# Optimization experiments

Hardware: AMD Instinct MI355X
Metric: run time of the kernel (lower is better)

The kernel has to match this reference:

```python
import jax, jax.numpy as jnp
import numpy as np

GRID = 64  # 64x64 key grid -> K = 4096


def setup_inputs() -> dict:
    key = jax.random.key(0)
    k1, k2, k3, k4 = jax.random.split(key, 4)
    B, H, Q, K, D = 2, 8, 2048, GRID * GRID, 128
    queries = jax.random.normal(k1, (B, H, Q, D), dtype=jnp.float32)
    keys = jax.random.normal(k2, (B, H, K, D), dtype=jnp.float32)
    # integer (x, y) query positions on the grid
    pos = jax.random.randint(k3, (B, Q, 2), 0, GRID).astype(jnp.int64)
    # relative bias table per head, offsets in [-(GRID-1), GRID-1]
    rel_bias = jax.random.normal(k4, (H, 2 * GRID - 1, 2 * GRID - 1), dtype=jnp.float32)
    # key grid coordinates (row-major flattened 64x64 grid)
    ar = jnp.arange(K)
    grid_x = (ar % GRID).astype(jnp.int64)
    grid_y = (ar // GRID).astype(jnp.int64)
    return {"queries": queries, "keys": keys, "pos": pos, "rel_bias": rel_bias,
            "grid_x": grid_x, "grid_y": grid_y}


def reference(queries, keys, pos, rel_bias, grid_x, grid_y):
    # queries: [B,H,Q,D], keys: [B,H,K,D], pos: [B,Q,2] int,
    # rel_bias: [H,2G-1,2G-1], grid_x/grid_y: [K] int
    D = queries.shape[-1]
    scale = jnp.asarray(1.0 / np.sqrt(D), dtype=queries.dtype)
    scores = jnp.einsum('bhqd,bhkd->bhqk', queries, keys) * scale  # [B,H,Q,K]
    Hb, Wb = rel_bias.shape[-2], rel_bias.shape[-1]
    cy, cx = (Hb - 1) // 2, (Wb - 1) // 2
    # relative offsets, shifted to table indices: [B,Q,K]
    dy = grid_y[None, None, :] - pos[:, :, 1][:, :, None] + cy
    dx = grid_x[None, None, :] - pos[:, :, 0][:, :, None] + cx
    dy = jnp.clip(dy, 0, Hb - 1)
    dx = jnp.clip(dx, 0, Wb - 1)
    flat = (dy * Wb + dx).astype(jnp.int32)  # [B,Q,K]
    # gather per-head bias: [H, B, Q, K] -> [B, H, Q, K]
    bias = jnp.take(rel_bias.reshape(rel_bias.shape[0], -1), flat, axis=1)
    scores = scores + jnp.transpose(bias, (1, 0, 2, 3))
    return jax.nn.softmax(scores, axis=-1)
```

## Files before the change

kernel.cpp:

```cpp
#include <hip/hip_runtime.h>
#include <hip/hip_bf16.h>

typedef __attribute__((ext_vector_type(8))) short short8;
typedef __attribute__((ext_vector_type(4))) float f32x4;

constexpr int Bn = 2, Hn = 8, NQ = 2048, NK = 4096, Dd = 128, Wt = 127;
constexpr int QT = 64, KT = 64;
constexpr int SPLITS = 8, K1_TILES = 8, NC2 = 4;
constexpr int NROWS = Bn * Hn * NQ;
constexpr float SCALE = 0.08838834764831845f;
constexpr float LOG2E = 1.4426950408889634f;
constexpr float S2 = SCALE * LOG2E;
constexpr float BSHIFT = 12.0f * LOG2E;

constexpr size_t WS_SUMS = 0;
constexpr size_t WS_K = 1u << 20;
constexpr size_t WS_Q = WS_K + (size_t)Bn * Hn * NK * Dd * 2;
constexpr size_t WS_B = WS_Q + (size_t)Bn * Hn * NQ * Dd * 2;

constexpr int KELEM = Bn * Hn * NK * Dd;
constexpr int QELEM = Bn * Hn * NQ * Dd;
constexpr int BELEM = Hn * Wt * Wt;
constexpr int KBLK = KELEM / 2048;
constexpr int QBLK = QELEM / 2048;
constexpr int BBLK = (BELEM + 2047) / 2048;

__device__ __forceinline__ short bf16r(float f) {
  union { float f; unsigned u; } v; v.f = f;
  unsigned r = v.u + 0x7fffu + ((v.u >> 16) & 1u);
  return (short)(r >> 16);
}

__device__ __forceinline__ float exp2hw(float x) {
  float r;
  asm("v_exp_f32 %0, %1" : "=v"(r) : "v"(x));
  return r;
}

__global__ __launch_bounds__(256)
void prep_kernel(const float* __restrict__ Km, const float* __restrict__ Qm,
                 const float* __restrict__ Bias, short* __restrict__ wsK,
                 short* __restrict__ wsQ, float* __restrict__ wsB) {
  const int bid = blockIdx.x, tid = threadIdx.x;
  if (bid < KBLK) {
    size_t i = (size_t)bid * 2048 + tid * 8;
    float4 f0 = *(const float4*)(Km + i);
    float4 f1 = *(const float4*)(Km + i + 4);
    short8 v;
    v[0] = bf16r(f0.x); v[1] = bf16r(f0.y); v[2] = bf16r(f0.z); v[3] = bf16r(f0.w);
    v[4] = bf16r(f1.x); v[5] = bf16r(f1.y); v[6] = bf16r(f1.z); v[7] = bf16r(f1.w);
    *(short8*)(wsK + i) = v;
  } else if (bid < KBLK + QBLK) {
    size_t i = (size_t)(bid - KBLK) * 2048 + tid * 8;
    float4 f0 = *(const float4*)(Qm + i);
    float4 f1 = *(const float4*)(Qm + i + 4);
    short8 v;
    v[0] = bf16r(f0.x); v[1] = bf16r(f0.y); v[2] = bf16r(f0.z); v[3] = bf16r(f0.w);
    v[4] = bf16r(f1.x); v[5] = bf16r(f1.y); v[6] = bf16r(f1.z); v[7] = bf16r(f1.w);
    *(short8*)(wsQ + i) = v;
  } else {
    int i = (bid - KBLK - QBLK) * 2048 + tid * 8;
#pragma unroll
    for (int j = 0; j < 8; j++)
      if (i + j < BELEM) wsB[i + j] = Bias[i + j] * LOG2E - BSHIFT;
  }
}

__device__ __forceinline__ void stage_async(int tid, const short* __restrict__ kp,
                                            int kt0, short* buf) {
  const int wave = tid >> 6, lane = tid & 63;
#pragma unroll
  for (int c = 0; c < 4; c++) {
    const int db = c * 4096 + wave * 1024 + lane * 16;
    const int row = db >> 8;
    const int scol = ((db >> 4) & 15) ^ (row & 7);
    const short* src = kp + (size_t)(kt0 + row) * Dd + scol * 8;
    __builtin_amdgcn_global_load_lds(
        (const __attribute__((address_space(1))) void*)src,
        (__attribute__((address_space(3))) void*)(buf + ((c * 4096 + wave * 1024) >> 1)),
        16, 0, 0);
  }
}

__device__ __forceinline__ short8 loadKfrag(const short* buf, int f, int kc,
                                            int l15, int g) {
  const int krow = f * 16 + l15;
  const int byte = (krow << 8) + ((((kc << 2) + g) ^ (krow & 7)) << 4);
  return *(const short8*)((const char*)buf + byte);
}

__global__ __launch_bounds__(256, 4)
void rga_sum_kernel(const short* __restrict__ wsK, const short* __restrict__ wsQ,
                    const int* __restrict__ Pos, const float* __restrict__ wsB,
                    float* __restrict__ sums) {
  __shared__ short lds[2][KT * Dd];
  const int tid = threadIdx.x, wave = tid >> 6, lane = tid & 63;
  const int l15 = lane & 15, g = lane >> 4;
  const int x0 = blockIdx.x;
  const int x = (x0 & 7) * 512 + (x0 >> 3);
  const int qt = x & 31, split = (x >> 5) & 7, bh = x >> 8;
  const int b = bh >> 3, h = bh & 7;

  const short* kp = wsK + (size_t)bh * NK * Dd;
  const short* qp = wsQ + (size_t)bh * NQ * Dd;
  const float* bp = wsB + (size_t)h * Wt * Wt;

  const int q = qt * QT + wave * 16 + l15;
  short8 qfrag[4];
#pragma unroll
  for (int kc = 0; kc < 4; kc++)
    qfrag[kc] = *(const short8*)(qp + (size_t)q * Dd + kc * 32 + g * 8);
  const int pxo = 63 - Pos[((size_t)b * NQ + q) * 2 + 0];
  const int pyo = 63 - Pos[((size_t)b * NQ + q) * 2 + 1];

  const int kt0 = split * (NK / SPLITS);
  stage_async(tid, kp, kt0, lds[0]);
  __syncthreads();

  float ksum = 0.f;
  for (int t = 0; t < K1_TILES; t++) {
    const int kt = kt0 + t * KT;
    if (t + 1 < K1_TILES) stage_async(tid, kp, kt + KT, lds[(t + 1) & 1]);
    const short* buf = lds[t & 1];
    const float* brow = bp + ((kt >> 6) + pyo) * Wt + pxo;
#pragma unroll
    for (int f = 0; f < 4; f++) {
      f32x4 acc = {0.f, 0.f, 0.f, 0.f};
#pragma unroll
      for (int kc = 0; kc < 4; kc++)
        acc = __builtin_amdgcn_mfma_f32_16x16x32_bf16(loadKfrag(buf, f, kc, l15, g),
                                                      qfrag[kc], acc, 0, 0, 0);
      const int gx0 = f * 16 + g * 4;
#pragma unroll
      for (int j = 0; j < 4; j++)
        ksum += exp2hw(acc[j] * S2 + brow[gx0 + j]);
    }
    __syncthreads();
  }
  ksum += __shfl_xor(ksum, 16, 64);
  ksum += __shfl_xor(ksum, 32, 64);
  if (lane < 16) sums[(size_t)split * NROWS + (size_t)bh * NQ + q] = ksum;
}

__global__ __launch_bounds__(256, 4)
void rga_out_kernel(const short* __restrict__ wsK, const short* __restrict__ wsQ,
                    const int* __restrict__ Pos, const float* __restrict__ wsB,
                    const float* __restrict__ sums, float* __restrict__ Out) {
  __shared__ short lds[2][KT * Dd];
  const int tid = threadIdx.x, wave = tid >> 6, lane = tid & 63;
  const int l15 = lane & 15, g = lane >> 4;
  const int x0 = blockIdx.x;
  const int x = (x0 & 7) * 1024 + (x0 >> 3);
  const int qt = x & 31, kc4 = (x >> 5) & 15, bh = x >> 9;
  const int b = bh >> 3, h = bh & 7;

  const short* kp = wsK + (size_t)bh * NK * Dd;
  const short* qp = wsQ + (size_t)bh * NQ * Dd;
  const float* bp = wsB + (size_t)h * Wt * Wt;

  const int q = qt * QT + wave * 16 + l15;
  short8 qfrag[4];
#pragma unroll
  for (int kc = 0; kc < 4; kc++)
    qfrag[kc] = *(const short8*)(qp + (size_t)q * Dd + kc * 32 + g * 8);
  const int pxo = 63 - Pos[((size_t)b * NQ + q) * 2 + 0];
  const int pyo = 63 - Pos[((size_t)b * NQ + q) * 2 + 1];

  float lsum = 0.f;
#pragma unroll
  for (int s = 0; s < SPLITS; s++) lsum += sums[(size_t)s * NROWS + (size_t)bh * NQ + q];
  const float rl = 1.0f / lsum;

  float* orow = Out + ((size_t)bh * NQ + q) * NK;
  const int kbase = kc4 * (KT * NC2);
  stage_async(tid, kp, kbase, lds[0]);
  __syncthreads();

  for (int t = 0; t < NC2; t++) {
    const int kt = kbase + t * KT;
    if (t + 1 < NC2) stage_async(tid, kp, kt + KT, lds[(t + 1) & 1]);
    const short* buf = lds[t & 1];
    const float* brow = bp + ((kt >> 6) + pyo) * Wt + pxo;
#pragma unroll
    for (int f = 0; f < 4; f++) {
      f32x4 acc = {0.f, 0.f, 0.f, 0.f};
#pragma unroll
      for (int kc = 0; kc < 4; kc++)
        acc = __builtin_amdgcn_mfma_f32_16x16x32_bf16(loadKfrag(buf, f, kc, l15, g),
                                                      qfrag[kc], acc, 0, 0, 0);
      const int gx0 = f * 16 + g * 4;
      f32x4 v;
      v[0] = exp2hw(acc[0] * S2 + brow[gx0 + 0]) * rl;
      v[1] = exp2hw(acc[1] * S2 + brow[gx0 + 1]) * rl;
      v[2] = exp2hw(acc[2] * S2 + brow[gx0 + 2]) * rl;
      v[3] = exp2hw(acc[3] * S2 + brow[gx0 + 3]) * rl;
      __builtin_nontemporal_store(v, (f32x4*)(orow + kt + gx0));
    }
    __syncthreads();
  }
}

extern "C" void kernel_launch(void* const* d_in, const int* in_sizes, int n_in,
                              void* d_out, int out_size, void* d_ws, size_t ws_size,
                              hipStream_t stream) {
  const float* q = (const float*)d_in[0];
  const float* k = (const float*)d_in[1];
  const int* pos = (const int*)d_in[2];
  const float* bias = (const float*)d_in[3];
  float* out = (float*)d_out;

  char* wsc = (char*)d_ws;
  float* sums = (float*)(wsc + WS_SUMS);
  short* wsK = (short*)(wsc + WS_K);
  short* wsQ = (short*)(wsc + WS_Q);
  float* wsB = (float*)(wsc + WS_B);

  hipLaunchKernelGGL(prep_kernel, dim3(KBLK + QBLK + BBLK), dim3(256), 0, stream,
                     k, q, bias, wsK, wsQ, wsB);
  hipLaunchKernelGGL(rga_sum_kernel, dim3(Bn * Hn * 32 * SPLITS), dim3(256), 0,
                     stream, wsK, wsQ, pos, wsB, sums);
  hipLaunchKernelGGL(rga_out_kernel, dim3(Bn * Hn * 32 * (NK / (KT * NC2))),
                     dim3(256), 0, stream, wsK, wsQ, pos, wsB, sums, out);
}
```

Measured before the change: 248.4 us.

## Drop LDS staging; each wave owns 64 queries and loads K fragments directly

Removes the shared-memory double-buffered K staging and block-level barriers. Each wave now processes 64 query rows (4 MFMA row groups) against its own K range, loading K fragments straight from global memory and reusing each K fragment across four query groups in registers. This aims to cut LDS traffic and synchronisation, but raises register pressure (launch bounds lowered to 3 blocks) and makes K reads per-wave global loads that rely on cache hits.

```diff
diff --git a/kernel.cpp b/kernel.cpp
--- a/kernel.cpp
+++ b/kernel.cpp
@@ -5,8 +5,7 @@
 typedef __attribute__((ext_vector_type(4))) float f32x4;
 
 constexpr int Bn = 2, Hn = 8, NQ = 2048, NK = 4096, Dd = 128, Wt = 127;
-constexpr int QT = 64, KT = 64;
-constexpr int SPLITS = 8, K1_TILES = 8, NC2 = 4;
+constexpr int SPLITS = 8;
 constexpr int NROWS = Bn * Hn * NQ;
 constexpr float SCALE = 0.08838834764831845f;
 constexpr float LOG2E = 1.4426950408889634f;
@@ -66,137 +65,149 @@
   }
 }
 
-__device__ __forceinline__ void stage_async(int tid, const short* __restrict__ kp,
-                                            int kt0, short* buf) {
-  const int wave = tid >> 6, lane = tid & 63;
-#pragma unroll
-  for (int c = 0; c < 4; c++) {
-    const int db = c * 4096 + wave * 1024 + lane * 16;
-    const int row = db >> 8;
-    const int scol = ((db >> 4) & 15) ^ (row & 7);
-    const short* src = kp + (size_t)(kt0 + row) * Dd + scol * 8;
-    __builtin_amdgcn_global_load_lds(
-        (const __attribute__((address_space(1))) void*)src,
-        (__attribute__((address_space(3))) void*)(buf + ((c * 4096 + wave * 1024) >> 1)),
-        16, 0, 0);
-  }
-}
-
-__device__ __forceinline__ short8 loadKfrag(const short* buf, int f, int kc,
-                                            int l15, int g) {
-  const int krow = f * 16 + l15;
-  const int byte = (krow << 8) + ((((kc << 2) + g) ^ (krow & 7)) << 4);
-  return *(const short8*)((const char*)buf + byte);
-}
-
-__global__ __launch_bounds__(256, 4)
+__global__ __launch_bounds__(256, 3)
 void rga_sum_kernel(const short* __restrict__ wsK, const short* __restrict__ wsQ,
                     const int* __restrict__ Pos, const float* __restrict__ wsB,
                     float* __restrict__ sums) {
-  __shared__ short lds[2][KT * Dd];
   const int tid = threadIdx.x, wave = tid >> 6, lane = tid & 63;
   const int l15 = lane & 15, g = lane >> 4;
-  const int x0 = blockIdx.x;
-  const int x = (x0 & 7) * 512 + (x0 >> 3);
-  const int qt = x & 31, split = (x >> 5) & 7, bh = x >> 8;
+  const int blk = (blockIdx.x & 7) * 128 + (blockIdx.x >> 3);
+  const int x = blk * 4 + wave;
+  const int split = x & 7, qu = (x >> 3) & 31, bh = x >> 8;
   const int b = bh >> 3, h = bh & 7;
 
   const short* kp = wsK + (size_t)bh * NK * Dd;
   const short* qp = wsQ + (size_t)bh * NQ * Dd;
   const float* bp = wsB + (size_t)h * Wt * Wt;
-
-  const int q = qt * QT + wave * 16 + l15;
-  short8 qfrag[4];
-#pragma unroll
-  for (int kc = 0; kc < 4; kc++)
-    qfrag[kc] = *(const short8*)(qp + (size_t)q * Dd + kc * 32 + g * 8);
-  const int pxo = 63 - Pos[((size_t)b * NQ + q) * 2 + 0];
-  const int pyo = 63 - Pos[((size_t)b * NQ + q) * 2 + 1];
-
+  const int q0 = qu * 64;
+
+  short8 qf[4][4];
+#pragma unroll
+  for (int r = 0; r < 4; r++)
+#pragma unroll
+    for (int kc = 0; kc < 4; kc++)
+      qf[r][kc] = *(const short8*)(qp + (size_t)(q0 + r * 16 + l15) * Dd + kc * 32 + g * 8);
+
+  int pxo[4], pyo[4];
+#pragma unroll
+  for (int r = 0; r < 4; r++) {
+    int2 p = ((const int2*)Pos)[(size_t)b * NQ + q0 + r * 16 + l15];
+    pxo[r] = 63 - p.x; pyo[r] = 63 - p.y;
+  }
+
+  float ks[4] = {0.f, 0.f, 0.f, 0.f};
   const int kt0 = split * (NK / SPLITS);
-  stage_async(tid, kp, kt0, lds[0]);
-  __syncthreads();
-
-  float ksum = 0.f;
-  for (int t = 0; t < K1_TILES; t++) {
-    const int kt = kt0 + t * KT;
-    if (t + 1 < K1_TILES) stage_async(tid, kp, kt + KT, lds[(t + 1) & 1]);
-    const short* buf = lds[t & 1];
-    const float* brow = bp + ((kt >> 6) + pyo) * Wt + pxo;
+  for (int t = 0; t < 8; t++) {
+    const int kt = kt0 + t * 64;
+    const int gy = kt >> 6;
+    const float* brow[4];
+#pragma unroll
+    for (int r = 0; r < 4; r++) brow[r] = bp + (gy + pyo[r]) * Wt + pxo[r];
 #pragma unroll
     for (int f = 0; f < 4; f++) {
-      f32x4 acc = {0.f, 0.f, 0.f, 0.f};
-#pragma unroll
-      for (int kc = 0; kc < 4; kc++)
-        acc = __builtin_amdgcn_mfma_f32_16x16x32_bf16(loadKfrag(buf, f, kc, l15, g),
-                                                      qfrag[kc], acc, 0, 0, 0);
+      short8 kf[4];
+#pragma unroll
+      for (int kc = 0; kc < 4; kc++)
+        kf[kc] = *(const short8*)(kp + (size_t)(kt + f * 16 + l15) * Dd + kc * 32 + g * 8);
+      f32x4 acc[4] = {{0.f,0.f,0.f,0.f},{0.f,0.f,0.f,0.f},{0.f,0.f,0.f,0.f},{0.f,0.f,0.f,0.f}};
+#pragma unroll
+      for (int kc = 0; kc < 4; kc++)
+#pragma unroll
+        for (int r = 0; r < 4; r++)
+          acc[r] = __builtin_amdgcn_mfma_f32_16x16x32_bf16(kf[kc], qf[r][kc], acc[r], 0, 0, 0);
       const int gx0 = f * 16 + g * 4;
 #pragma unroll
-      for (int j = 0; j < 4; j++)
-        ksum += exp2hw(acc[j] * S2 + brow[gx0 + j]);
+      for (int r = 0; r < 4; r++)
+#pragma unroll
+        for (int j = 0; j < 4; j++)
+          ks[r] += exp2hw(acc[r][j] * S2 + brow[r][gx0 + j]);
     }
-    __syncthreads();
-  }
-  ksum += __shfl_xor(ksum, 16, 64);
-  ksum += __shfl_xor(ksum, 32, 64);
-  if (lane < 16) sums[(size_t)split * NROWS + (size_t)bh * NQ + q] = ksum;
-}
-
-__global__ __launch_bounds__(256, 4)
+  }
+#pragma unroll
+  for (int r = 0; r < 4; r++) {
+    ks[r] += __shfl_xor(ks[r], 16, 64);
+    ks[r] += __shfl_xor(ks[r], 32, 64);
+  }
+  if (lane < 16) {
+#pragma unroll
+    for (int r = 0; r < 4; r++)
+      sums[(size_t)split * NROWS + (size_t)bh * NQ + q0 + r * 16 + l15] = ks[r];
+  }
+}
+
+__global__ __launch_bounds__(256, 3)
 void rga_out_kernel(const short* __restrict__ wsK, const short* __restrict__ wsQ,
                     const int* __restrict__ Pos, const float* __restrict__ wsB,
                     const float* __restrict__ sums, float* __restrict__ Out) {
-  __shared__ short lds[2][KT * Dd];
   const int tid = threadIdx.x, wave = tid >> 6, lane = tid & 63;
   const int l15 = lane & 15, g = lane >> 4;
-  const int x0 = blockIdx.x;
-  const int x = (x0 & 7) * 1024 + (x0 >> 3);
-  const int qt = x & 31, kc4 = (x >> 5) & 15, bh = x >> 9;
+  const int blk = (blockIdx.x & 7) * 256 + (blockIdx.x >> 3);
+  const int x = blk * 4 + wave;
+  const int ku = x & 15, qu = (x >> 4) & 31, bh = x >> 9;
   const int b = bh >> 3, h = bh & 7;
 
   const short* kp = wsK + (size_t)bh * NK * Dd;
   const short* qp = wsQ + (size_t)bh * NQ * Dd;
   const float* bp = wsB + (size_t)h * Wt * Wt;
-
-  const int q = qt * QT + wave * 16 + l15;
-  short8 qfrag[4];
-#pragma unroll
-  for (int kc = 0; kc < 4; kc++)
-    qfrag[kc] = *(const short8*)(qp + (size_t)q * Dd + kc * 32 + g * 8);
-  const int pxo = 63 - Pos[((size_t)b * NQ + q) * 2 + 0];
-  const int pyo = 63 - Pos[((size_t)b * NQ + q) * 2 + 1];
-
-  float lsum = 0.f;
-#pragma unroll
-  for (int s = 0; s < SPLITS; s++) lsum += sums[(size_t)s * NROWS + (size_t)bh * NQ + q];
-  const float rl = 1.0f / lsum;
-
-  float* orow = Out + ((size_t)bh * NQ + q) * NK;
-  const int kbase = kc4 * (KT * NC2);
-  stage_async(tid, kp, kbase, lds[0]);
-  __syncthreads();
-
-  for (int t = 0; t < NC2; t++) {
-    const int kt = kbase + t * KT;
-    if (t + 1 < NC2) stage_async(tid, kp, kt + KT, lds[(t + 1) & 1]);
-    const short* buf = lds[t & 1];
-    const float* brow = bp + ((kt >> 6) + pyo) * Wt + pxo;
+  const int q0 = qu * 64;
+
+  short8 qf[4][4];
+#pragma unroll
+  for (int r = 0; r < 4; r++)
+#pragma unroll
+    for (int kc = 0; kc < 4; kc++)
+      qf[r][kc] = *(const short8*)(qp + (size_t)(q0 + r * 16 + l15) * Dd + kc * 32 + g * 8);
+
+  int pxo[4], pyo[4];
+#pragma unroll
+  for (int r = 0; r < 4; r++) {
+    int2 p = ((const int2*)Pos)[(size_t)b * NQ + q0 + r * 16 + l15];
+    pxo[r] = 63 - p.x; pyo[r] = 63 - p.y;
+  }
+
+  float rl[4];
+#pragma unroll
+  for (int r = 0; r < 4; r++) {
+    float ls = 0.f;
+#pragma unroll
+    for (int s = 0; s < SPLITS; s++)
+      ls += sums[(size_t)s * NROWS + (size_t)bh * NQ + q0 + r * 16 + l15];
+    rl[r] = 1.0f / ls;
+  }
+
+  float* orow[4];
+#pragma unroll
+  for (int r = 0; r < 4; r++)
+    orow[r] = Out + ((size_t)bh * NQ + q0 + r * 16 + l15) * NK;
+
+  for (int t = 0; t < 4; t++) {
+    const int kt = ku * 256 + t * 64;
+    const int gy = kt >> 6;
+    const float* brow[4];
+#pragma unroll
+    for (int r = 0; r < 4; r++) brow[r] = bp + (gy + pyo[r]) * Wt + pxo[r];
 #pragma unroll
     for (int f = 0; f < 4; f++) {
-      f32x4 acc = {0.f, 0.f, 0.f, 0.f};
-#pragma unroll
-      for (int kc = 0; kc < 4; kc++)
-        acc = __builtin_amdgcn_mfma_f32_16x16x32_bf16(loadKfrag(buf, f, kc, l15, g),
-                                                      qfrag[kc], acc, 0, 0, 0);
+      short8 kf[4];
+#pragma unroll
+      for (int kc = 0; kc < 4; kc++)
+        kf[kc] = *(const short8*)(kp + (size_t)(kt + f * 16 + l15) * Dd + kc * 32 + g * 8);
+      f32x4 acc[4] = {{0.f,0.f,0.f,0.f},{0.f,0.f,0.f,0.f},{0.f,0.f,0.f,0.f},{0.f,0.f,0.f,0.f}};
+#pragma unroll
+      for (int kc = 0; kc < 4; kc++)
+#pragma unroll
+        for (int r = 0; r < 4; r++)
+          acc[r] = __builtin_amdgcn_mfma_f32_16x16x32_bf16(kf[kc], qf[r][kc], acc[r], 0, 0, 0);
       const int gx0 = f * 16 + g * 4;
-      f32x4 v;
-      v[0] = exp2hw(acc[0] * S2 + brow[gx0 + 0]) * rl;
-      v[1] = exp2hw(acc[1] * S2 + brow[gx0 + 1]) * rl;
-      v[2] = exp2hw(acc[2] * S2 + brow[gx0 + 2]) * rl;
-      v[3] = exp2hw(acc[3] * S2 + brow[gx0 + 3]) * rl;
-      __builtin_nontemporal_store(v, (f32x4*)(orow + kt + gx0));
+#pragma unroll
+      for (int r = 0; r < 4; r++) {
+        f32x4 v;
+#pragma unroll
+        for (int j = 0; j < 4; j++)
+          v[j] = exp2hw(acc[r][j] * S2 + brow[r][gx0 + j]) * rl[r];
+        __builtin_nontemporal_store(v, (f32x4*)(orow[r] + kt + gx0));
+      }
     }
-    __syncthreads();
   }
 }
 
@@ -217,8 +228,8 @@
 
   hipLaunchKernelGGL(prep_kernel, dim3(KBLK + QBLK + BBLK), dim3(256), 0, stream,
                      k, q, bias, wsK, wsQ, wsB);
-  hipLaunchKernelGGL(rga_sum_kernel, dim3(Bn * Hn * 32 * SPLITS), dim3(256), 0,
-                     stream, wsK, wsQ, pos, wsB, sums);
-  hipLaunchKernelGGL(rga_out_kernel, dim3(Bn * Hn * 32 * (NK / (KT * NC2))),
-                     dim3(256), 0, stream, wsK, wsQ, pos, wsB, sums, out);
-}
+  hipLaunchKernelGGL(rga_sum_kernel, dim3(1024), dim3(256), 0, stream,
+                     wsK, wsQ, pos, wsB, sums);
+  hipLaunchKernelGGL(rga_out_kernel, dim3(2048), dim3(256), 0, stream,
+                     wsK, wsQ, pos, wsB, sums, out);
+}
```

Result: slower. 333.6 us (+34.3%).
